# Performance work log

Hardware: AMD Instinct MI355X
Metric: run time of the kernel (lower is better)

## Reference

```python
import jax, jax.numpy as jnp
import numpy as np

NUM_HEADS = 12


def _rel_indices(H, W):
    # [N, N, 3] with channels (dx, dy, dx^2+dy^2), N = H*W
    indx = jnp.arange(W)[None, :] - jnp.arange(W)[:, None]          # [W, W]
    indx = jnp.tile(indx, (H, H))                                    # [N, N]
    indy = jnp.arange(H)[None, :] - jnp.arange(H)[:, None]          # [H, H]
    indy = jnp.repeat(jnp.repeat(indy, W, axis=0), W, axis=1)        # [N, N]
    indd = indx ** 2 + indy ** 2
    return jnp.stack([indx, indy, indd], axis=-1).astype(jnp.float32)


def setup_inputs() -> dict:
    key = jax.random.key(0)
    ks = jax.random.split(key, 8)
    B, N, C = 16, 576, 768
    std = 0.02
    return {
        "x": jax.random.normal(ks[0], (B, N, C), dtype=jnp.float32),
        "Wq": jax.random.normal(ks[1], (C, C), dtype=jnp.float32) * std,
        "Wk": jax.random.normal(ks[2], (C, C), dtype=jnp.float32) * std,
        "Wv": jax.random.normal(ks[3], (C, C), dtype=jnp.float32) * std,
        "Wproj": jax.random.normal(ks[4], (C, C), dtype=jnp.float32) * std,
        "bproj": jnp.zeros((C,), dtype=jnp.float32),
        "pos_w": jax.random.normal(ks[5], (3, NUM_HEADS), dtype=jnp.float32) * std,
        "pos_b": jnp.zeros((NUM_HEADS,), dtype=jnp.float32),
        "gating": jnp.ones((NUM_HEADS,), dtype=jnp.float32),
        "H": 24,
        "W": 24,
    }


def reference(x, Wq, Wk, Wv, Wproj, bproj, pos_w, pos_b, gating, H, W):
    B, N, C = x.shape
    h = gating.shape[0]
    d = C // h
    scale = d ** (-0.5)

    def heads(t):  # [B,N,C] -> [B,h,N,d]
        return t.reshape(B, N, h, d).transpose(0, 2, 1, 3)

    q = heads(x @ Wq)
    k = heads(x @ Wk)
    v = heads(x @ Wv)

    # content scores: [B,h,N,N]
    patch_score = jax.nn.softmax(jnp.einsum('bhnd,bhmd->bhnm', q, k) * scale, axis=-1)

    # positional scores: shared across batch, [h,N,N]
    rel = _rel_indices(H, W)                      # [N,N,3]
    pos_score = jnp.einsum('nmc,ch->hnm', rel, pos_w) + pos_b[:, None, None]
    pos_score = jax.nn.softmax(pos_score, axis=-1)

    gate = jax.nn.sigmoid(gating)[None, :, None, None]  # [1,h,1,1]
    attn = (1.0 - gate) * patch_score + gate * pos_score[None]
    attn = attn / jnp.sum(attn, axis=-1, keepdims=True)

    out = jnp.einsum('bhnm,bhmd->bhnd', attn, v)         # [B,h,N,d]
    out = out.transpose(0, 2, 1, 3).reshape(B, N, C)
    return out @ Wproj + bproj
```

## Files before the change

kernel.cpp:

```cpp
#include <hip/hip_runtime.h>
#include <math.h>

#define B_ 16
#define N_ 576
#define C_ 768
#define NH 12
#define D_ 64
#define STR 68
#define QKV 2304

typedef unsigned short u16;
typedef __bf16 bf16x8 __attribute__((ext_vector_type(8)));
typedef float f32x4 __attribute__((ext_vector_type(4)));

__device__ __forceinline__ u16 f2bf(float f) {
    unsigned u = __builtin_bit_cast(unsigned, f);
    unsigned r = (u + 0x7FFFu + ((u >> 16) & 1u)) >> 16;
    return (u16)r;
}

__device__ __forceinline__ bf16x8 ldsF8u(const u16* p) {
    union { uint2 u[2]; bf16x8 v; } t;
    t.u[0] = *(const uint2*)p;
    t.u[1] = *(const uint2*)(p + 4);
    return t.v;
}
__device__ __forceinline__ bf16x8 ldsF8a(const u16* p) {
    union { uint4 u; bf16x8 v; } t;
    t.u = *(const uint4*)p;
    return t.v;
}

__device__ __forceinline__ void gload16(const u16* g, u16* l) {
    __builtin_amdgcn_global_load_lds(
        (const __attribute__((address_space(1))) void*)g,
        (__attribute__((address_space(3))) void*)l,
        16, 0, 0);
}

__global__ __launch_bounds__(256)
void conv_x_kernel(const float* __restrict__ x, u16* __restrict__ xb)
{
    int i = blockIdx.x * 256 + threadIdx.x;
    float4 v = ((const float4*)x)[i];
    u16 o[4] = {f2bf(v.x), f2bf(v.y), f2bf(v.z), f2bf(v.w)};
    *(uint2*)&xb[(size_t)i * 4] = *(const uint2*)o;
}

__global__ __launch_bounds__(256)
void transpose_w_kernel(const float* __restrict__ src, u16* __restrict__ dst)
{
    __shared__ float t[32][33];
    const int bx = blockIdx.x * 32, by = blockIdx.y * 32;
    const int tx = threadIdx.x & 31, ty = threadIdx.x >> 5;
#pragma unroll
    for (int i = 0; i < 32; i += 8)
        t[ty + i][tx] = src[(size_t)(by + ty + i) * C_ + bx + tx];
    __syncthreads();
#pragma unroll
    for (int i = 0; i < 32; i += 8)
        dst[(size_t)(bx + ty + i) * C_ + by + tx] = f2bf(t[tx][ty + i]);
}

__global__ __launch_bounds__(256)
void transpose_v_kernel(const u16* __restrict__ qkvb, u16* __restrict__ vtb)
{
    __shared__ u16 t[64 * 72];
    const int n0 = blockIdx.x * 64;
    const int bh = blockIdx.y;
    const int b = bh / NH, h = bh % NH;
    const int tid = threadIdx.x;
    const u16* src = qkvb + ((size_t)b * N_ + n0) * QKV + 2 * C_ + h * D_;
#pragma unroll
    for (int p = 0; p < 2; ++p) {
        int idx = p * 256 + tid;
        int r = idx >> 3, c = (idx & 7) << 3;
        *(uint4*)&t[r * 72 + c] = *(const uint4*)(src + (size_t)r * QKV + c);
    }
    __syncthreads();
    u16* dst = vtb + (size_t)bh * D_ * N_ + n0;
#pragma unroll
    for (int p = 0; p < 2; ++p) {
        int idx = p * 256 + tid;
        int dd = idx >> 3, n8 = (idx & 7) << 3;
        u16 o[8];
#pragma unroll
        for (int j = 0; j < 8; ++j) o[j] = t[(n8 + j) * 72 + dd];
        *(uint4*)(dst + (size_t)dd * N_ + n8) = *(const uint4*)o;
    }
}

__global__ __launch_bounds__(256)
void mfma_gemm(const u16* __restrict__ A,
               const u16* __restrict__ BT,
               const float* __restrict__ bias,
               float* __restrict__ out,
               u16* __restrict__ outb,
               int ldo, int mode)
{
    const int K = C_;
    __shared__ __align__(16) u16 As[128 * 64];
    __shared__ __align__(16) u16 Bs[128 * 64];
    const int tid = threadIdx.x;
    const int wave = tid >> 6, lane = tid & 63;
    const int quad = lane >> 4, l16 = lane & 15;
    const int wy = wave >> 1, wx = wave & 1;
    const int tm = blockIdx.y * 128, tn = blockIdx.x * 128;

    const int lr = lane >> 3;
    const int sc = ((lane & 7) ^ lr) * 8;

    f32x4 acc[4][4];
#pragma unroll
    for (int i = 0; i < 4; ++i)
#pragma unroll
        for (int j = 0; j < 4; ++j)
            acc[i][j] = (f32x4){0.f, 0.f, 0.f, 0.f};

    for (int k0 = 0; k0 < K; k0 += 64) {
        __syncthreads();
#pragma unroll
        for (int t = 0; t < 4; ++t) {
            const int rg = wave * 32 + t * 8;
            gload16(A  + (size_t)(tm + rg + lr) * K + k0 + sc, &As[rg * 64]);
            gload16(BT + (size_t)(tn + rg + lr) * K + k0 + sc, &Bs[rg * 64]);
        }
        __syncthreads();

#pragma unroll
        for (int kh = 0; kh < 2; ++kh) {
            bf16x8 aA[4], bB[4];
#pragma unroll
            for (int i = 0; i < 4; ++i) {
                const int s = (kh * 4 + quad) ^ (l16 & 7);
                aA[i] = ldsF8a(&As[(wy * 64 + i * 16 + l16) * 64 + s * 8]);
            }
#pragma unroll
            for (int j = 0; j < 4; ++j) {
                const int s = (kh * 4 + quad) ^ (l16 & 7);
                bB[j] = ldsF8a(&Bs[(wx * 64 + j * 16 + l16) * 64 + s * 8]);
            }
#pragma unroll
            for (int i = 0; i < 4; ++i)
#pragma unroll
                for (int j = 0; j < 4; ++j)
                    acc[i][j] = __builtin_amdgcn_mfma_f32_16x16x32_bf16(aA[i], bB[j], acc[i][j], 0, 0, 0);
        }
    }

    if (mode == 0) {
#pragma unroll
        for (int i = 0; i < 4; ++i) {
#pragma unroll
            for (int r = 0; r < 4; ++r) {
                const int m = tm + wy * 64 + i * 16 + quad * 4 + r;
#pragma unroll
                for (int j = 0; j < 4; ++j) {
                    const int c = tn + wx * 64 + j * 16 + l16;
                    out[(size_t)m * ldo + c] = acc[i][j][r] + bias[c];
                }
            }
        }
    } else {
        const float scale = (tn < C_) ? 0.125f : 1.0f;
#pragma unroll
        for (int i = 0; i < 4; ++i) {
#pragma unroll
            for (int r = 0; r < 4; ++r) {
                const int m = tm + wy * 64 + i * 16 + quad * 4 + r;
#pragma unroll
                for (int j = 0; j < 4; ++j) {
                    const int c = tn + wx * 64 + j * 16 + l16;
                    outb[(size_t)m * ldo + c] = f2bf(acc[i][j][r] * scale);
                }
            }
        }
    }
}

__global__ __launch_bounds__(256)
void pos_softmax_kernel(const float* __restrict__ pos_w,
                        const float* __restrict__ pos_b,
                        const int* __restrict__ Hp,
                        const int* __restrict__ Wp,
                        u16* __restrict__ pos_out)
{
    const int n = blockIdx.x;
    const int hh = blockIdx.y;
    const int tid = threadIdx.x;
    __shared__ float srow[N_];
    __shared__ float wred[4];
    const int Ww = Wp[0];
    (void)Hp;
    const float w0 = pos_w[0 * NH + hh];
    const float w1 = pos_w[1 * NH + hh];
    const float w2 = pos_w[2 * NH + hh];
    const float bb = pos_b[hh];
    const int nx = n % Ww, ny = n / Ww;

    float lmax = -1e30f;
    for (int m = tid; m < N_; m += 256) {
        float dx = (float)((m % Ww) - nx);
        float dy = (float)((m / Ww) - ny);
        float sc = dx * w0 + dy * w1 + (dx * dx + dy * dy) * w2 + bb;
        srow[m] = sc;
        lmax = fmaxf(lmax, sc);
    }
#pragma unroll
    for (int off = 32; off; off >>= 1) lmax = fmaxf(lmax, __shfl_down(lmax, off, 64));
    if ((tid & 63) == 0) wred[tid >> 6] = lmax;
    __syncthreads();
    float M = fmaxf(fmaxf(wred[0], wred[1]), fmaxf(wred[2], wred[3]));
    __syncthreads();

    float lsum = 0.f;
    for (int m = tid; m < N_; m += 256) {
        float e = __expf(srow[m] - M);
        srow[m] = e;
        lsum += e;
    }
#pragma unroll
    for (int off = 32; off; off >>= 1) lsum += __shfl_down(lsum, off, 64);
    if ((tid & 63) == 0) wred[tid >> 6] = lsum;
    __syncthreads();
    float inv = 1.0f / (wred[0] + wred[1] + wred[2] + wred[3]);

    u16* op = pos_out + ((size_t)hh * N_ + n) * N_;
    for (int m = tid; m < N_; m += 256) op[m] = f2bf(srow[m] * inv);
}

__global__ __launch_bounds__(256)
void attn_kernel(const u16* __restrict__ qkvb,
                 const u16* __restrict__ vt,
                 const u16* __restrict__ pos,
                 const float* __restrict__ gating,
                 u16* __restrict__ ao)
{
    const int qt = blockIdx.x;
    const int bh = blockIdx.y;
    const int b = bh / NH, h = bh % NH;
    const int tid = threadIdx.x;
    const int wave = tid >> 6, lane = tid & 63;
    const int quad = lane >> 4, l16 = lane & 15;

    __shared__ u16 smem[4 * 64 * STR];
    u16* Kt = smem;
    u16* Vs = smem + 64 * STR;
    u16* Pp = smem + 2 * 64 * STR;
    u16* Pb = smem + 3 * 64 * STR;

    const u16* qptr  = qkvb + ((size_t)b * N_ + qt * 64) * QKV + h * D_;
    const u16* kbase = qkvb + (size_t)b * N_ * QKV + C_ + h * D_;
    const u16* vbase = vt + (size_t)bh * D_ * N_;
    const u16* pbase = pos + ((size_t)h * N_ + qt * 64) * N_;

    const int sr = tid >> 3;
    const int scol = (tid & 7) << 3;

#pragma unroll
    for (int p = 0; p < 2; ++p) {
        int r = p * 32 + sr;
        uint4 d = *(const uint4*)(qptr + (size_t)r * QKV + scol);
        *(uint2*)&Pb[r * STR + scol]     = make_uint2(d.x, d.y);
        *(uint2*)&Pb[r * STR + scol + 4] = make_uint2(d.z, d.w);
    }
    __syncthreads();

    const int arow = wave * 16 + l16;
    bf16x8 aq0 = ldsF8u(&Pb[arow * STR + quad * 8]);
    bf16x8 aq1 = ldsF8u(&Pb[arow * STR + 32 + quad * 8]);

    uint4 rk[2], rv[2], rp[2];
    auto loadT = [&](int m0) {
#pragma unroll
        for (int p = 0; p < 2; ++p) {
            int r = p * 32 + sr;
            rk[p] = *(const uint4*)(kbase + (size_t)(m0 + r) * QKV + scol);
            rv[p] = *(const uint4*)(vbase + (size_t)r * N_ + m0 + scol);
            rp[p] = *(const uint4*)(pbase + (size_t)r * N_ + m0 + scol);
        }
    };
    auto writeT = [&]() {
#pragma unroll
        for (int p = 0; p < 2; ++p) {
            int r = p * 32 + sr;
            *(uint2*)&Kt[r * STR + scol]     = make_uint2(rk[p].x, rk[p].y);
            *(uint2*)&Kt[r * STR + scol + 4] = make_uint2(rk[p].z, rk[p].w);
            *(uint2*)&Vs[r * STR + scol]     = make_uint2(rv[p].x, rv[p].y);
            *(uint2*)&Vs[r * STR + scol + 4] = make_uint2(rv[p].z, rv[p].w);
            *(uint2*)&Pp[r * STR + scol]     = make_uint2(rp[p].x, rp[p].y);
            *(uint2*)&Pp[r * STR + scol + 4] = make_uint2(rp[p].z, rp[p].w);
        }
    };

    loadT(0);

    f32x4 oc[4], op[4];
#pragma unroll
    for (int nt = 0; nt < 4; ++nt) {
        oc[nt] = (f32x4){0.f, 0.f, 0.f, 0.f};
        op[nt] = (f32x4){0.f, 0.f, 0.f, 0.f};
    }
    float lrun[4] = {0.f, 0.f, 0.f, 0.f};

    for (int mt = 0; mt < 9; ++mt) {
        __syncthreads();
        writeT();
        __syncthreads();
        if (mt < 8) loadT((mt + 1) * 64);

        f32x4 s[4];
#pragma unroll
        for (int nt = 0; nt < 4; ++nt) {
            bf16x8 b0 = ldsF8u(&Kt[(nt * 16 + l16) * STR + quad * 8]);
            bf16x8 b1 = ldsF8u(&Kt[(nt * 16 + l16) * STR + 32 + quad * 8]);
            f32x4 z = (f32x4){0.f, 0.f, 0.f, 0.f};
            z = __builtin_amdgcn_mfma_f32_16x16x32_bf16(aq0, b0, z, 0, 0, 0);
            z = __builtin_amdgcn_mfma_f32_16x16x32_bf16(aq1, b1, z, 0, 0, 0);
            s[nt] = z;
        }

#pragma unroll
        for (int r = 0; r < 4; ++r) {
            const int prow = (wave * 16 + quad * 4 + r) * STR;
            float e0 = __expf(s[0][r]);
            float e1 = __expf(s[1][r]);
            float e2 = __expf(s[2][r]);
            float e3 = __expf(s[3][r]);
            Pb[prow +  0 + l16] = f2bf(e0);
            Pb[prow + 16 + l16] = f2bf(e1);
            Pb[prow + 32 + l16] = f2bf(e2);
            Pb[prow + 48 + l16] = f2bf(e3);
            lrun[r] += (e0 + e1) + (e2 + e3);
        }
        asm volatile("s_waitcnt lgkmcnt(0)" ::: "memory");

#pragma unroll
        for (int ks = 0; ks < 2; ++ks) {
            bf16x8 ap   = ldsF8u(&Pb[arow * STR + ks * 32 + quad * 8]);
            bf16x8 apos = ldsF8u(&Pp[arow * STR + ks * 32 + quad * 8]);
#pragma unroll
            for (int nt = 0; nt < 4; ++nt) {
                bf16x8 bv = ldsF8u(&Vs[(nt * 16 + l16) * STR + ks * 32 + quad * 8]);
                oc[nt] = __builtin_amdgcn_mfma_f32_16x16x32_bf16(ap,   bv, oc[nt], 0, 0, 0);
                op[nt] = __builtin_amdgcn_mfma_f32_16x16x32_bf16(apos, bv, op[nt], 0, 0, 0);
            }
        }
    }

#pragma unroll
    for (int r = 0; r < 4; ++r) {
        lrun[r] += __shfl_xor(lrun[r], 1, 64);
        lrun[r] += __shfl_xor(lrun[r], 2, 64);
        lrun[r] += __shfl_xor(lrun[r], 4, 64);
        lrun[r] += __shfl_xor(lrun[r], 8, 64);
    }

    const float g = 1.f / (1.f + __expf(-gating[h]));
#pragma unroll
    for (int r = 0; r < 4; ++r) {
        const float sc = (1.f - g) / lrun[r];
        const int row = qt * 64 + wave * 16 + quad * 4 + r;
#pragma unroll
        for (int nt = 0; nt < 4; ++nt) {
            ao[((size_t)b * N_ + row) * C_ + h * D_ + nt * 16 + l16] =
                f2bf(oc[nt][r] * sc + g * op[nt][r]);
        }
    }
}

extern "C" void kernel_launch(void* const* d_in, const int* in_sizes, int n_in,
                              void* d_out, int out_size, void* d_ws, size_t ws_size,
                              hipStream_t stream)
{
    const float* x      = (const float*)d_in[0];
    const float* Wq     = (const float*)d_in[1];
    const float* Wk     = (const float*)d_in[2];
    const float* Wv     = (const float*)d_in[3];
    const float* Wproj  = (const float*)d_in[4];
    const float* bproj  = (const float*)d_in[5];
    const float* pos_w  = (const float*)d_in[6];
    const float* pos_b  = (const float*)d_in[7];
    const float* gating = (const float*)d_in[8];
    const int*   Hp     = (const int*)d_in[9];
    const int*   Wp     = (const int*)d_in[10];
    float* out = (float*)d_out;

    const size_t xe = (size_t)B_ * N_ * C_;
    const size_t we = (size_t)C_ * C_;
    const size_t qe = (size_t)B_ * N_ * QKV;
    const size_t pe = (size_t)NH * N_ * N_;
    u16* xb   = (u16*)d_ws;
    u16* wt   = xb + xe;
    u16* wtp  = wt + 3 * we;
    u16* qkvb = wtp + we;
    u16* vtb  = qkvb + qe;
    u16* posb = vtb + xe;
    u16* aob  = posb + pe;
    size_t need = (size_t)(3 * xe + 4 * we + qe + pe) * sizeof(u16);
    if (ws_size < need) return;

    conv_x_kernel<<<dim3((unsigned)(xe / 1024)), 256, 0, stream>>>(x, xb);
    dim3 tgrid(24, 24);
    transpose_w_kernel<<<tgrid, 256, 0, stream>>>(Wq, wt);
    transpose_w_kernel<<<tgrid, 256, 0, stream>>>(Wk, wt + we);
    transpose_w_kernel<<<tgrid, 256, 0, stream>>>(Wv, wt + 2 * we);
    transpose_w_kernel<<<tgrid, 256, 0, stream>>>(Wproj, wtp);

    mfma_gemm<<<dim3(18, 72), 256, 0, stream>>>(xb, wt, nullptr, nullptr,
                                                qkvb, QKV, 1);
    transpose_v_kernel<<<dim3(9, B_ * NH), 256, 0, stream>>>(qkvb, vtb);
    pos_softmax_kernel<<<dim3(N_, NH), 256, 0, stream>>>(pos_w, pos_b, Hp, Wp, posb);
    attn_kernel<<<dim3(9, B_ * NH), 256, 0, stream>>>(qkvb, vtb, posb, gating, aob);
    mfma_gemm<<<dim3(6, 72), 256, 0, stream>>>(aob, wtp, bproj, out,
                                               nullptr, C_, 0);
}
```

Baseline: 246.9 us.

## Factor positional softmax into separable x/y convolutions over V

```diff
diff --git a/kernel.cpp b/kernel.cpp
--- a/kernel.cpp
+++ b/kernel.cpp
@@ -6,6 +6,7 @@
 #define C_ 768
 #define NH 12
 #define D_ 64
+#define GW 24
 #define STR 68
 #define QKV 2304
 
@@ -17,6 +18,10 @@
     unsigned u = __builtin_bit_cast(unsigned, f);
     unsigned r = (u + 0x7FFFu + ((u >> 16) & 1u)) >> 16;
     return (u16)r;
+}
+__device__ __forceinline__ float bf2f(u16 b) {
+    unsigned u = ((unsigned)b) << 16;
+    return __builtin_bit_cast(float, u);
 }
 
 __device__ __forceinline__ bf16x8 ldsF8u(const u16* p) {
@@ -48,8 +53,13 @@
 }
 
 __global__ __launch_bounds__(256)
-void transpose_w_kernel(const float* __restrict__ src, u16* __restrict__ dst)
-{
+void transpose_w4_kernel(const float* __restrict__ w0, const float* __restrict__ w1,
+                         const float* __restrict__ w2, const float* __restrict__ w3,
+                         u16* __restrict__ dst_base)
+{
+    const float* srcs[4] = {w0, w1, w2, w3};
+    const float* src = srcs[blockIdx.z];
+    u16* dst = dst_base + (size_t)blockIdx.z * C_ * C_;
     __shared__ float t[32][33];
     const int bx = blockIdx.x * 32, by = blockIdx.y * 32;
     const int tx = threadIdx.x & 31, ty = threadIdx.x >> 5;
@@ -179,60 +189,124 @@
 }
 
 __global__ __launch_bounds__(256)
-void pos_softmax_kernel(const float* __restrict__ pos_w,
-                        const float* __restrict__ pos_b,
-                        const int* __restrict__ Hp,
-                        const int* __restrict__ Wp,
-                        u16* __restrict__ pos_out)
-{
-    const int n = blockIdx.x;
-    const int hh = blockIdx.y;
+void pos_stage1_kernel(const u16* __restrict__ qkvb,
+                       const float* __restrict__ pos_w,
+                       float* __restrict__ T1)
+{
+    const int bh = blockIdx.x;
+    const int b = bh / NH, h = bh % NH;
     const int tid = threadIdx.x;
-    __shared__ float srow[N_];
-    __shared__ float wred[4];
-    const int Ww = Wp[0];
-    (void)Hp;
-    const float w0 = pos_w[0 * NH + hh];
-    const float w1 = pos_w[1 * NH + hh];
-    const float w2 = pos_w[2 * NH + hh];
-    const float bb = pos_b[hh];
-    const int nx = n % Ww, ny = n / Ww;
-
-    float lmax = -1e30f;
-    for (int m = tid; m < N_; m += 256) {
-        float dx = (float)((m % Ww) - nx);
-        float dy = (float)((m / Ww) - ny);
-        float sc = dx * w0 + dy * w1 + (dx * dx + dy * dy) * w2 + bb;
-        srow[m] = sc;
-        lmax = fmaxf(lmax, sc);
-    }
-#pragma unroll
-    for (int off = 32; off; off >>= 1) lmax = fmaxf(lmax, __shfl_down(lmax, off, 64));
-    if ((tid & 63) == 0) wred[tid >> 6] = lmax;
-    __syncthreads();
-    float M = fmaxf(fmaxf(wred[0], wred[1]), fmaxf(wred[2], wred[3]));
-    __syncthreads();
-
-    float lsum = 0.f;
-    for (int m = tid; m < N_; m += 256) {
-        float e = __expf(srow[m] - M);
-        srow[m] = e;
-        lsum += e;
-    }
-#pragma unroll
-    for (int off = 32; off; off >>= 1) lsum += __shfl_down(lsum, off, 64);
-    if ((tid & 63) == 0) wred[tid >> 6] = lsum;
-    __syncthreads();
-    float inv = 1.0f / (wred[0] + wred[1] + wred[2] + wred[3]);
-
-    u16* op = pos_out + ((size_t)hh * N_ + n) * N_;
-    for (int m = tid; m < N_; m += 256) op[m] = f2bf(srow[m] * inv);
+    __shared__ float ey[47];
+    const float w1 = pos_w[NH + h], w2 = pos_w[2 * NH + h];
+
+    if (tid < 47) {
+        float dy = (float)(tid - 23);
+        ey[tid] = __expf(w1 * dy + w2 * dy * dy);
+    }
+    __syncthreads();
+    if (tid >= 192) return;
+    const int mx = tid >> 3, c = (tid & 7) << 3;
+    const u16* src = qkvb + (size_t)b * N_ * QKV + 2 * C_ + h * D_ + c;
+
+#pragma unroll
+    for (int np = 0; np < 3; ++np) {
+        float acc[8][8];
+#pragma unroll
+        for (int q = 0; q < 8; ++q)
+#pragma unroll
+            for (int j = 0; j < 8; ++j) acc[q][j] = 0.f;
+        for (int my = 0; my < GW; ++my) {
+            union { uint4 u; u16 s[8]; } d;
+            d.u = *(const uint4*)(src + (size_t)(my * GW + mx) * QKV);
+            float vf[8];
+#pragma unroll
+            for (int j = 0; j < 8; ++j) vf[j] = bf2f(d.s[j]);
+#pragma unroll
+            for (int q = 0; q < 8; ++q) {
+                float e = ey[my - (np * 8 + q) + 23];
+#pragma unroll
+                for (int j = 0; j < 8; ++j) acc[q][j] += e * vf[j];
+            }
+        }
+#pragma unroll
+        for (int q = 0; q < 8; ++q) {
+            const int ny = np * 8 + q;
+            float* dst = T1 + (((size_t)bh * GW + ny) * GW + mx) * D_ + c;
+            *(float4*)dst       = *(float4*)&acc[q][0];
+            *(float4*)(dst + 4) = *(float4*)&acc[q][4];
+        }
+    }
+}
+
+__global__ __launch_bounds__(256)
+void pos_stage2_kernel(const float* __restrict__ T1,
+                       const float* __restrict__ pos_w,
+                       const float* __restrict__ gating,
+                       u16* __restrict__ aob)
+{
+    const int bh = blockIdx.x;
+    const int ny = blockIdx.y;
+    const int b = bh / NH, h = bh % NH;
+    const int tid = threadIdx.x;
+    __shared__ float T1s[GW * D_];
+    __shared__ float ex[47];
+    __shared__ float SxA[GW];
+    __shared__ float Sy;
+    const float w0 = pos_w[h], w1 = pos_w[NH + h], w2 = pos_w[2 * NH + h];
+
+    const float* tsrc = T1 + ((size_t)bh * GW + ny) * GW * D_;
+#pragma unroll
+    for (int i = 0; i < 2; ++i) {
+        int idx = i * 256 + tid;
+        if (idx < 384) ((float4*)T1s)[idx] = ((const float4*)tsrc)[idx];
+    }
+    if (tid < 47) {
+        float dx = (float)(tid - 23);
+        ex[tid] = __expf(w0 * dx + w2 * dx * dx);
+    }
+    if (tid == 192) {
+        float s = 0.f;
+        for (int my = 0; my < GW; ++my) {
+            float dy = (float)(my - ny);
+            s += __expf(w1 * dy + w2 * dy * dy);
+        }
+        Sy = s;
+    }
+    __syncthreads();
+    if (tid < GW) {
+        float s = 0.f;
+        for (int mx = 0; mx < GW; ++mx) s += ex[mx - tid + 23];
+        SxA[tid] = s;
+    }
+    __syncthreads();
+    if (tid >= 192) return;
+    const int nx = tid >> 3, c = (tid & 7) << 3;
+
+    float acc[8];
+#pragma unroll
+    for (int j = 0; j < 8; ++j) acc[j] = 0.f;
+    for (int mx = 0; mx < GW; ++mx) {
+        float e = ex[mx - nx + 23];
+        float4 t0 = *(float4*)&T1s[mx * D_ + c];
+        float4 t1 = *(float4*)&T1s[mx * D_ + c + 4];
+        acc[0] += e * t0.x; acc[1] += e * t0.y; acc[2] += e * t0.z; acc[3] += e * t0.w;
+        acc[4] += e * t1.x; acc[5] += e * t1.y; acc[6] += e * t1.z; acc[7] += e * t1.w;
+    }
+    const float g = 1.f / (1.f + __expf(-gating[h]));
+    const float sc = g / (SxA[nx] * Sy);
+    const int n = ny * GW + nx;
+    u16* dst = aob + ((size_t)b * N_ + n) * C_ + h * D_ + c;
+    u16 cur[8];
+    *(uint4*)cur = *(const uint4*)dst;
+    u16 o[8];
+#pragma unroll
+    for (int j = 0; j < 8; ++j) o[j] = f2bf(bf2f(cur[j]) + sc * acc[j]);
+    *(uint4*)dst = *(const uint4*)o;
 }
 
 __global__ __launch_bounds__(256)
 void attn_kernel(const u16* __restrict__ qkvb,
                  const u16* __restrict__ vt,
-                 const u16* __restrict__ pos,
                  const float* __restrict__ gating,
                  u16* __restrict__ ao)
 {
@@ -243,16 +317,14 @@
     const int wave = tid >> 6, lane = tid & 63;
     const int quad = lane >> 4, l16 = lane & 15;
 
-    __shared__ u16 smem[4 * 64 * STR];
+    __shared__ u16 smem[3 * 64 * STR];
     u16* Kt = smem;
     u16* Vs = smem + 64 * STR;
-    u16* Pp = smem + 2 * 64 * STR;
-    u16* Pb = smem + 3 * 64 * STR;
+    u16* Pb = smem + 2 * 64 * STR;
 
     const u16* qptr  = qkvb + ((size_t)b * N_ + qt * 64) * QKV + h * D_;
     const u16* kbase = qkvb + (size_t)b * N_ * QKV + C_ + h * D_;
     const u16* vbase = vt + (size_t)bh * D_ * N_;
-    const u16* pbase = pos + ((size_t)h * N_ + qt * 64) * N_;
 
     const int sr = tid >> 3;
     const int scol = (tid & 7) << 3;
@@ -270,14 +342,13 @@
     bf16x8 aq0 = ldsF8u(&Pb[arow * STR + quad * 8]);
     bf16x8 aq1 = ldsF8u(&Pb[arow * STR + 32 + quad * 8]);
 
-    uint4 rk[2], rv[2], rp[2];
+    uint4 rk[2], rv[2];
     auto loadT = [&](int m0) {
 #pragma unroll
         for (int p = 0; p < 2; ++p) {
             int r = p * 32 + sr;
             rk[p] = *(const uint4*)(kbase + (size_t)(m0 + r) * QKV + scol);
             rv[p] = *(const uint4*)(vbase + (size_t)r * N_ + m0 + scol);
-            rp[p] = *(const uint4*)(pbase + (size_t)r * N_ + m0 + scol);
         }
     };
     auto writeT = [&]() {
@@ -288,19 +359,15 @@
             *(uint2*)&Kt[r * STR + scol + 4] = make_uint2(rk[p].z, rk[p].w);
             *(uint2*)&Vs[r * STR + scol]     = make_uint2(rv[p].x, rv[p].y);
             *(uint2*)&Vs[r * STR + scol + 4] = make_uint2(rv[p].z, rv[p].w);
-            *(uint2*)&Pp[r * STR + scol]     = make_uint2(rp[p].x, rp[p].y);
-            *(uint2*)&Pp[r * STR + scol + 4] = make_uint2(rp[p].z, rp[p].w);
         }
     };
 
     loadT(0);
 
-    f32x4 oc[4], op[4];
-#pragma unroll
-    for (int nt = 0; nt < 4; ++nt) {
+    f32x4 oc[4];
+#pragma unroll
+    for (int nt = 0; nt < 4; ++nt)
         oc[nt] = (f32x4){0.f, 0.f, 0.f, 0.f};
-        op[nt] = (f32x4){0.f, 0.f, 0.f, 0.f};
-    }
     float lrun[4] = {0.f, 0.f, 0.f, 0.f};
 
     for (int mt = 0; mt < 9; ++mt) {
@@ -337,13 +404,11 @@
 
 #pragma unroll
         for (int ks = 0; ks < 2; ++ks) {
-            bf16x8 ap   = ldsF8u(&Pb[arow * STR + ks * 32 + quad * 8]);
-            bf16x8 apos = ldsF8u(&Pp[arow * STR + ks * 32 + quad * 8]);
+            bf16x8 ap = ldsF8u(&Pb[arow * STR + ks * 32 + quad * 8]);
 #pragma unroll
             for (int nt = 0; nt < 4; ++nt) {
                 bf16x8 bv = ldsF8u(&Vs[(nt * 16 + l16) * STR + ks * 32 + quad * 8]);
-                oc[nt] = __builtin_amdgcn_mfma_f32_16x16x32_bf16(ap,   bv, oc[nt], 0, 0, 0);
-                op[nt] = __builtin_amdgcn_mfma_f32_16x16x32_bf16(apos, bv, op[nt], 0, 0, 0);
+                oc[nt] = __builtin_amdgcn_mfma_f32_16x16x32_bf16(ap, bv, oc[nt], 0, 0, 0);
             }
         }
     }
@@ -364,7 +429,7 @@
 #pragma unroll
         for (int nt = 0; nt < 4; ++nt) {
             ao[((size_t)b * N_ + row) * C_ + h * D_ + nt * 16 + l16] =
-                f2bf(oc[nt][r] * sc + g * op[nt][r]);
+                f2bf(oc[nt][r] * sc);
         }
     }
 }
@@ -380,38 +445,31 @@
     const float* Wproj  = (const float*)d_in[4];
     const float* bproj  = (const float*)d_in[5];
     const float* pos_w  = (const float*)d_in[6];
-    const float* pos_b  = (const float*)d_in[7];
     const float* gating = (const float*)d_in[8];
-    const int*   Hp     = (const int*)d_in[9];
-    const int*   Wp     = (const int*)d_in[10];
     float* out = (float*)d_out;
 
     const size_t xe = (size_t)B_ * N_ * C_;
     const size_t we = (size_t)C_ * C_;
     const size_t qe = (size_t)B_ * N_ * QKV;
-    const size_t pe = (size_t)NH * N_ * N_;
     u16* xb   = (u16*)d_ws;
     u16* wt   = xb + xe;
-    u16* wtp  = wt + 3 * we;
-    u16* qkvb = wtp + we;
+    u16* qkvb = wt + 4 * we;
     u16* vtb  = qkvb + qe;
-    u16* posb = vtb + xe;
-    u16* aob  = posb + pe;
-    size_t need = (size_t)(3 * xe + 4 * we + qe + pe) * sizeof(u16);
+    u16* aob  = vtb + xe;
+    float* T1 = (float*)(aob + xe);
+    size_t need = (size_t)(3 * xe + 4 * we + qe) * sizeof(u16)
+                + (size_t)B_ * NH * GW * GW * D_ * sizeof(float);
     if (ws_size < need) return;
 
     conv_x_kernel<<<dim3((unsigned)(xe / 1024)), 256, 0, stream>>>(x, xb);
-    dim3 tgrid(24, 24);
-    transpose_w_kernel<<<tgrid, 256, 0, stream>>>(Wq, wt);
-    transpose_w_kernel<<<tgrid, 256, 0, stream>>>(Wk, wt + we);
-    transpose_w_kernel<<<tgrid, 256, 0, stream>>>(Wv, wt + 2 * we);
-    transpose_w_kernel<<<tgrid, 256, 0, stream>>>(Wproj, wtp);
+    transpose_w4_kernel<<<dim3(24, 24, 4), 256, 0, stream>>>(Wq, Wk, Wv, Wproj, wt);
 
     mfma_gemm<<<dim3(18, 72), 256, 0, stream>>>(xb, wt, nullptr, nullptr,
                                                 qkvb, QKV, 1);
     transpose_v_kernel<<<dim3(9, B_ * NH), 256, 0, stream>>>(qkvb, vtb);
-    pos_softmax_kernel<<<dim3(N_, NH), 256, 0, stream>>>(pos_w, pos_b, Hp, Wp, posb);
-    attn_kernel<<<dim3(9, B_ * NH), 256, 0, stream>>>(qkvb, vtb, posb, gating, aob);
-    mfma_gemm<<<dim3(6, 72), 256, 0, stream>>>(aob, wtp, bproj, out,
+    pos_stage1_kernel<<<dim3(B_ * NH), 256, 0, stream>>>(qkvb, pos_w, T1);
+    attn_kernel<<<dim3(9, B_ * NH), 256, 0, stream>>>(qkvb, vtb, gating, aob);
+    pos_stage2_kernel<<<dim3(B_ * NH, GW), 256, 0, stream>>>(T1, pos_w, gating, aob);
+    mfma_gemm<<<dim3(6, 72), 256, 0, stream>>>(aob, wt + 3 * we, bproj, out,
                                                nullptr, C_, 0);
 }
```

Result: slower. 258.1 us (+4.6%).
